# Performance work log

Hardware: AMD Instinct MI355X
Metric: run time of the kernel (lower is better)

Reference implementation:

```python
import jax, jax.numpy as jnp
import numpy as np

BITS = 4
PACK = 32 // BITS  # 8 nibbles per int32
GROUP = 128
MASK = (1 << BITS) - 1


def _dequant(qweight, qzeros, scales):
    # qweight: [K//8, N] int32, nibbles packed along K (input) dim
    # qzeros : [G, N//8] int32, nibbles packed along N (output) dim
    # scales : [G, N] float
    shifts = jnp.arange(PACK, dtype=jnp.int32) * BITS  # [8]
    Kp, N = qweight.shape
    G = scales.shape[0]
    # unpack weights along input dim -> [K, N]
    w = (qweight[:, None, :] >> shifts[None, :, None]) & MASK  # [K//8, 8, N]
    w = w.reshape(Kp * PACK, N).astype(scales.dtype)
    # unpack zeros along output dim -> [G, N]
    z = (qzeros[:, :, None] >> shifts[None, None, :]) & MASK  # [G, N//8, 8]
    z = z.reshape(G, N).astype(scales.dtype) + 1.0  # GPTQ +1 zero offset
    # broadcast per-group zero/scale over GROUP consecutive input rows
    z_full = jnp.repeat(z, GROUP, axis=0)       # [K, N]
    s_full = jnp.repeat(scales, GROUP, axis=0)  # [K, N]
    return (w - z_full) * s_full  # [K, N]


def setup_inputs() -> dict:
    key = jax.random.key(0)
    k1, k2, k3, k4 = jax.random.split(key, 4)
    K, N, T = 4096, 11008, 8192
    x = jax.random.normal(k1, (T, K), dtype=jnp.float32)
    qweight = jax.random.randint(k2, (K // PACK, N), 0, 2147483647, dtype=jnp.int32)
    qzeros = jax.random.randint(k3, (K // GROUP, N // PACK), 0, 2147483647, dtype=jnp.int32)
    scales = jax.random.uniform(k4, (K // GROUP, N), dtype=jnp.float32) * 0.01
    return {"x": x, "qweight": qweight, "qzeros": qzeros, "scales": scales}


def reference(x, qweight, qzeros, scales):
    W = _dequant(qweight, qzeros, scales)  # [K, N]
    return x @ W  # [T, N]
```

## Files before the change

### kernel.cpp

```cpp
#include <hip/hip_runtime.h>
#include <hip/hip_bf16.h>
#include <cstdint>
#include <cstddef>


#define K_DIM 4096
#define N_DIM 11008
#define GROUP_SZ 128
#define KB (K_DIM * 2)
#define NTILES_K (K_DIM / 64)

typedef __bf16 bf16x8_t __attribute__((ext_vector_type(8)));
typedef float f32x4_t __attribute__((ext_vector_type(4)));

__device__ __forceinline__ void async_copy16(const void* g, void* l) {
    __builtin_amdgcn_global_load_lds((const __attribute__((address_space(1))) void*)g,
                                     (__attribute__((address_space(3))) void*)l,
                                     16, 0, 0);
}

__global__ __launch_bounds__(256) void convert_x_kernel(const float* __restrict__ x,
                                                        __bf16* __restrict__ xb,
                                                        long total,
                                                        unsigned* __restrict__ counter) {
    if (counter && blockIdx.x == 0 && threadIdx.x == 0) counter[0] = 0u;
    long i = ((long)blockIdx.x * 256 + threadIdx.x) * 8;
    if (i >= total) return;
    const float4* p = (const float4*)(x + i);
    float4 u = p[0], v = p[1];
    bf16x8_t o;
    o[0] = (__bf16)u.x; o[1] = (__bf16)u.y; o[2] = (__bf16)u.z; o[3] = (__bf16)u.w;
    o[4] = (__bf16)v.x; o[5] = (__bf16)v.y; o[6] = (__bf16)v.z; o[7] = (__bf16)v.w;
    *(bf16x8_t*)(xb + i) = o;
}

__global__ __launch_bounds__(256) void dequant_kernel(const int* __restrict__ qw,
                                                      const int* __restrict__ qz,
                                                      const float* __restrict__ sc,
                                                      __bf16* __restrict__ Wt) {
    __shared__ __align__(16) __bf16 dqT[128 * 136];
    __shared__ float dqS[128];
    __shared__ float dqB[128];
    const int n0 = blockIdx.x * 128;
    const int g  = blockIdx.y;
    const int t  = threadIdx.x;

    if (t < 128) {
        int n = n0 + t;
        float s = sc[(size_t)g * N_DIM + n];
        int z = (qz[(size_t)g * (N_DIM / 8) + (n >> 3)] >> ((n & 7) * 4)) & 15;
        dqS[t] = s;
        dqB[t] = -(float)(z + 1) * s;
    }
    __syncthreads();

#pragma unroll
    for (int it = 0; it < 8; ++it) {
        int wi  = it * 256 + t;
        int row = wi >> 7;
        int col = wi & 127;
        int q = qw[(size_t)(g * 16 + row) * N_DIM + n0 + col];
        float s = dqS[col], b = dqB[col];
        bf16x8_t v;
#pragma unroll
        for (int j = 0; j < 8; ++j) {
            float w = (float)((q >> (4 * j)) & 15);
            v[j] = (__bf16)fmaf(w, s, b);
        }
        *(bf16x8_t*)(&dqT[col * 136 + row * 8]) = v;
    }
    __syncthreads();

    int n_loc = t & 127, half = t >> 7;
    const __bf16* src = &dqT[n_loc * 136 + half * 64];
    __bf16* dst = Wt + (size_t)(n0 + n_loc) * K_DIM + g * GROUP_SZ + half * 64;
#pragma unroll
    for (int i = 0; i < 8; ++i)
        *(bf16x8_t*)(dst + i * 8) = *(const bf16x8_t*)(src + i * 8);
}

__device__ __forceinline__ void map_tile(int vid, int mtiles, int ntiles,
                                         int& mt, int& nt) {
    if ((mtiles & 15) == 0) {
        const int bandsz = 16 * ntiles;
        const int band = vid / bandsz, rem = vid % bandsz;
        nt = rem >> 4;
        mt = (band << 4) + (rem & 15);
    } else {
        mt = vid % mtiles;
        nt = vid / mtiles;
    }
}

__global__ __launch_bounds__(512, 2) void gemm256_kernel(const __bf16* __restrict__ A,
                                                         const __bf16* __restrict__ Bt,
                                                         float* __restrict__ C,
                                                         int mtiles, int ntiles,
                                                         unsigned* counter, int ntotal) {
    __shared__ __align__(16) char ldsA[2][256 * 128];
    __shared__ __align__(16) char ldsB[2][256 * 128];
    __shared__ int sVid;
    const int tid = threadIdx.x;

    int srcA[2], srcB[2], dstA[2], dstB[2];
#pragma unroll
    for (int q = 0; q < 2; ++q) {
        const int f = q * 512 + tid;
        const int r = f >> 3, c = f & 7;
        const int swz = (c * 16) ^ ((r & 7) << 4);
        const int Ra = r + (r & 64);
        const int Rb = r + (r & ~31);
        srcA[q] = Ra * KB + swz;  dstA[q] = Ra * 128 + c * 16;
        srcB[q] = Rb * KB + swz;  dstB[q] = Rb * 128 + c * 16;
    }

    const int lane = tid & 63;
    const int wid = tid >> 6;
    const int wm = wid >> 2, wn = wid & 3;
    const int lr = lane & 15, lq = lane >> 4;
    const int kOff0 = (lq * 16) ^ ((lr & 7) << 4);
    const int kOff1 = (64 + lq * 16) ^ ((lr & 7) << 4);
    const int aRowBase = wm * 128 + lr;
    const int bRowBase = wn * 64 + lr;

    bf16x8_t aF[4][2], bF[4][2];
    f32x4_t acc[8][4];

#define GL_A(AP, KT, BUFS, ROFF) do {                                                      \
    async_copy16((AP) + (size_t)(KT) * 128 + (ROFF) * KB + srcA[0],                        \
                 &ldsA[BUFS][(ROFF) * 128] + dstA[0]);                                     \
    async_copy16((AP) + (size_t)(KT) * 128 + (ROFF) * KB + srcA[1],                        \
                 &ldsA[BUFS][(ROFF) * 128] + dstA[1]);                                     \
} while (0)
#define GL_B(BP, KT, BUFS, ROFF) do {                                                      \
    async_copy16((BP) + (size_t)(KT) * 128 + (ROFF) * KB + srcB[0],                        \
                 &ldsB[BUFS][(ROFF) * 128] + dstB[0]);                                     \
    async_copy16((BP) + (size_t)(KT) * 128 + (ROFF) * KB + srcB[1],                        \
                 &ldsB[BUFS][(ROFF) * 128] + dstB[1]);                                     \
} while (0)
#define READ_A(MQ, BUFC) do {                                                              \
    _Pragma("unroll") for (int i = 0; i < 4; ++i) {                                        \
        const char* _p = &ldsA[BUFC][(aRowBase + (MQ) * 64 + i * 16) * 128];               \
        aF[i][0] = *(const bf16x8_t*)(_p + kOff0);                                         \
        aF[i][1] = *(const bf16x8_t*)(_p + kOff1);                                         \
    }                                                                                      \
} while (0)
#define READ_B(NQ, BUFC) do {                                                              \
    _Pragma("unroll") for (int j = 0; j < 2; ++j) {                                        \
        const char* _p = &ldsB[BUFC][(bRowBase + ((NQ) * 2 + j) * 16) * 128];              \
        bF[(NQ) * 2 + j][0] = *(const bf16x8_t*)(_p + kOff0);                              \
        bF[(NQ) * 2 + j][1] = *(const bf16x8_t*)(_p + kOff1);                              \
    }                                                                                      \
} while (0)
#define MFMA_QUAD(MQ, NQ) do {                                                             \
    _Pragma("unroll") for (int kk = 0; kk < 2; ++kk)                                       \
    _Pragma("unroll") for (int i = 0; i < 4; ++i)                                          \
    _Pragma("unroll") for (int j = 0; j < 2; ++j)                                          \
        acc[(MQ) * 4 + i][(NQ) * 2 + j] = __builtin_amdgcn_mfma_f32_16x16x32_bf16(         \
            aF[i][kk], bF[(NQ) * 2 + j][kk], acc[(MQ) * 4 + i][(NQ) * 2 + j], 0, 0, 0);    \
} while (0)
#define BARRIER() asm volatile("s_barrier" ::: "memory")
#define VMCNT4()  asm volatile("s_waitcnt vmcnt(4)" ::: "memory")
#define VMCNT0()  asm volatile("s_waitcnt vmcnt(0)" ::: "memory")

#define KTILE(AP, BP, BUFC, KTS) do {                                                      \
    READ_A(0, BUFC); READ_B(0, BUFC);                                                      \
    GL_A(AP, KTS, (BUFC) ^ 1, 0);                                                          \
    VMCNT4(); BARRIER();                                                                   \
    MFMA_QUAD(0, 0);                                                                       \
    READ_B(1, BUFC);                                                                       \
    GL_B(BP, KTS, (BUFC) ^ 1, 0);                                                          \
    VMCNT4(); BARRIER();                                                                   \
    MFMA_QUAD(0, 1);                                                                       \
    READ_A(1, BUFC);                                                                       \
    GL_B(BP, KTS, (BUFC) ^ 1, 32);                                                         \
    BARRIER();                                                                             \
    MFMA_QUAD(1, 1);                                                                       \
    GL_A(AP, KTS, (BUFC) ^ 1, 64);                                                         \
    VMCNT4(); BARRIER();                                                                   \
    MFMA_QUAD(1, 0);                                                                       \
} while (0)

#define KTILE_LAST(NAP, NBP, HAVE) do {                                                    \
    READ_A(0, 1); READ_B(0, 1);                                                            \
    if (HAVE) { GL_A(NAP, 0, 0, 0); VMCNT4(); } else { VMCNT0(); }                         \
    BARRIER();                                                                             \
    MFMA_QUAD(0, 0);                                                                       \
    READ_B(1, 1);                                                                          \
    if (HAVE) GL_B(NBP, 0, 0, 0);                                                          \
    VMCNT4(); BARRIER();                                                                   \
    MFMA_QUAD(0, 1);                                                                       \
    READ_A(1, 1);                                                                          \
    if (HAVE) GL_B(NBP, 0, 0, 32);                                                         \
    BARRIER();                                                                             \
    MFMA_QUAD(1, 1);                                                                       \
    if (HAVE) GL_A(NAP, 0, 0, 64);                                                         \
    VMCNT4(); BARRIER();                                                                   \
    MFMA_QUAD(1, 0);                                                                       \
} while (0)

    int vid;
    if (counter) {
        if (tid == 0) sVid = (int)atomicAdd(counter, 1u);
        __syncthreads();
        vid = sVid;
    } else {
        const int nwg = gridDim.x, bid = blockIdx.x;
        vid = (nwg & 7) ? bid : ((bid & 7) * (nwg >> 3) + (bid >> 3));
    }

    bool first = true;
    while (vid < ntotal) {
        int mt, nt;
        map_tile(vid, mtiles, ntiles, mt, nt);
        const char* aPanel = (const char*)A + (size_t)mt * 256 * KB;
        const char* bPanel = (const char*)Bt + (size_t)nt * 256 * KB;

        if (first) {
            GL_A(aPanel, 0, 0, 0); GL_B(bPanel, 0, 0, 0);
            GL_B(bPanel, 0, 0, 32); GL_A(aPanel, 0, 0, 64);
            VMCNT4(); BARRIER();
            first = false;
        }

#pragma unroll
        for (int m = 0; m < 8; ++m)
#pragma unroll
            for (int n = 0; n < 4; ++n)
                acc[m][n] = (f32x4_t){0.f, 0.f, 0.f, 0.f};

#pragma unroll 1
        for (int kt = 0; kt < NTILES_K - 2; kt += 2) {
            KTILE(aPanel, bPanel, 0, kt + 1);
            KTILE(aPanel, bPanel, 1, kt + 2);
        }
        KTILE(aPanel, bPanel, 0, NTILES_K - 1);

        int nvid;
        if (counter) {
            if (tid == 0) sVid = (int)atomicAdd(counter, 1u);
            __syncthreads();
            nvid = sVid;
        } else {
            nvid = ntotal;
        }
        const bool have = nvid < ntotal;
        const char* naP = aPanel;
        const char* nbP = bPanel;
        if (have) {
            int nmt, nnt;
            map_tile(nvid, mtiles, ntiles, nmt, nnt);
            naP = (const char*)A + (size_t)nmt * 256 * KB;
            nbP = (const char*)Bt + (size_t)nnt * 256 * KB;
        }
        KTILE_LAST(naP, nbP, have);

#pragma unroll
        for (int m = 0; m < 8; ++m) {
            const size_t gr = (size_t)mt * 256 + wm * 128 + m * 16 + lq * 4;
#pragma unroll
            for (int n = 0; n < 4; ++n) {
                const size_t gc = (size_t)nt * 256 + wn * 64 + n * 16 + lr;
                float* cp = C + gr * N_DIM + gc;
#pragma unroll
                for (int rg = 0; rg < 4; ++rg)
                    cp[(size_t)rg * N_DIM] = acc[m][n][rg];
            }
        }

        vid = nvid;
    }
}

__global__ __launch_bounds__(256) void fallback_kernel(const float* __restrict__ x,
                                                       const int* __restrict__ qw,
                                                       const int* __restrict__ qz,
                                                       const float* __restrict__ sc,
                                                       float* __restrict__ out) {
    __shared__ float xrow[K_DIM];
    const int t = blockIdx.y;
    const int n = blockIdx.x * 256 + threadIdx.x;
    for (int i = threadIdx.x; i < K_DIM; i += 256)
        xrow[i] = x[(size_t)t * K_DIM + i];
    __syncthreads();
    if (n >= N_DIM) return;
    float acc = 0.f;
    for (int g = 0; g < K_DIM / GROUP_SZ; ++g) {
        float s = sc[(size_t)g * N_DIM + n];
        int z = (qz[(size_t)g * (N_DIM / 8) + (n >> 3)] >> ((n & 7) * 4)) & 15;
        float b = -(float)(z + 1) * s;
        for (int kp = g * 16; kp < g * 16 + 16; ++kp) {
            int q = qw[(size_t)kp * N_DIM + n];
#pragma unroll
            for (int j = 0; j < 8; ++j) {
                float w = (float)((q >> (4 * j)) & 15);
                acc = fmaf(xrow[kp * 8 + j], fmaf(w, s, b), acc);
            }
        }
    }
    out[(size_t)t * N_DIM + n] = acc;
}

extern "C" void kernel_launch(void* const* d_in, const int* in_sizes, int n_in,
                              void* d_out, int out_size, void* d_ws, size_t ws_size,
                              hipStream_t stream) {
    const float* x  = (const float*)d_in[0];
    const int*   qw = (const int*)d_in[1];
    const int*   qz = (const int*)d_in[2];
    const float* sc = (const float*)d_in[3];
    float* out = (float*)d_out;

    const long T = (long)in_sizes[0] / K_DIM;
    const size_t xb_bytes = (size_t)T * K_DIM * sizeof(__bf16);
    const size_t wt_bytes = (size_t)N_DIM * K_DIM * sizeof(__bf16);
    const size_t cnt_off  = (xb_bytes + wt_bytes + 255) & ~(size_t)255;

    if (ws_size >= xb_bytes + wt_bytes && (T % 256) == 0) {
        __bf16* xb = (__bf16*)d_ws;
        __bf16* Wt = (__bf16*)((char*)d_ws + xb_bytes);
        unsigned* counter = (ws_size >= cnt_off + 256)
                          ? (unsigned*)((char*)d_ws + cnt_off) : nullptr;
        long total = T * K_DIM;
        long nthr = total / 8;
        convert_x_kernel<<<dim3((unsigned)((nthr + 255) / 256)), dim3(256), 0, stream>>>(x, xb, total, counter);
        dequant_kernel<<<dim3(N_DIM / 128, K_DIM / GROUP_SZ), dim3(256), 0, stream>>>(qw, qz, sc, Wt);
        const int mtiles = (int)(T / 256);
        const int ntiles = N_DIM / 256;
        const int ntotal = mtiles * ntiles;
        const unsigned grid = counter ? 256u : (unsigned)ntotal;
        gemm256_kernel<<<dim3(grid), dim3(512), 0, stream>>>(xb, Wt, out, mtiles, ntiles, counter, ntotal);
    } else {
        fallback_kernel<<<dim3(N_DIM / 256 + 1, (unsigned)T), dim3(256), 0, stream>>>(x, qw, qz, sc, out);
    }
}
```

Baseline: 729.0 us.

## Double-buffer MFMA fragments and prefetch next k-tile fragments across tile boundary

Splits the A/B register fragments into separate low/high and b0/b1 sets so LDS reads for the next quadrant, and for the next k-tile's first quadrant, are issued before the current MFMA block rather than after a barrier. This hides LDS read latency behind MFMA work and reorders the quadrant sequence to (0,0),(0,1),(1,0),(1,1). In exchange it raises VGPR use, which risks spills or lower occupancy, and it changes barrier/vmcnt placement, including a weaker wait in the last tile.

```diff
diff --git a/kernel.cpp b/kernel.cpp
--- a/kernel.cpp
+++ b/kernel.cpp
@@ -123,7 +123,7 @@
     const int aRowBase = wm * 128 + lr;
     const int bRowBase = wn * 64 + lr;
 
-    bf16x8_t aF[4][2], bF[4][2];
+    bf16x8_t aLo[4][2], aHi[4][2], b0[2][2], b1[2][2];
     f32x4_t acc[8][4];
 
 #define GL_A(AP, KT, BUFS, ROFF) do {                                                      \
@@ -138,65 +138,70 @@
     async_copy16((BP) + (size_t)(KT) * 128 + (ROFF) * KB + srcB[1],                        \
                  &ldsB[BUFS][(ROFF) * 128] + dstB[1]);                                     \
 } while (0)
-#define READ_A(MQ, BUFC) do {                                                              \
+#define READ_AX(DST, MQ, BUF) do {                                                         \
     _Pragma("unroll") for (int i = 0; i < 4; ++i) {                                        \
-        const char* _p = &ldsA[BUFC][(aRowBase + (MQ) * 64 + i * 16) * 128];               \
-        aF[i][0] = *(const bf16x8_t*)(_p + kOff0);                                         \
-        aF[i][1] = *(const bf16x8_t*)(_p + kOff1);                                         \
+        const char* _p = &ldsA[BUF][(aRowBase + (MQ) * 64 + i * 16) * 128];                \
+        DST[i][0] = *(const bf16x8_t*)(_p + kOff0);                                        \
+        DST[i][1] = *(const bf16x8_t*)(_p + kOff1);                                        \
     }                                                                                      \
 } while (0)
-#define READ_B(NQ, BUFC) do {                                                              \
+#define READ_BX(DST, NQ, BUF) do {                                                         \
     _Pragma("unroll") for (int j = 0; j < 2; ++j) {                                        \
-        const char* _p = &ldsB[BUFC][(bRowBase + ((NQ) * 2 + j) * 16) * 128];              \
-        bF[(NQ) * 2 + j][0] = *(const bf16x8_t*)(_p + kOff0);                              \
-        bF[(NQ) * 2 + j][1] = *(const bf16x8_t*)(_p + kOff1);                              \
+        const char* _p = &ldsB[BUF][(bRowBase + ((NQ) * 2 + j) * 16) * 128];               \
+        DST[j][0] = *(const bf16x8_t*)(_p + kOff0);                                        \
+        DST[j][1] = *(const bf16x8_t*)(_p + kOff1);                                        \
     }                                                                                      \
 } while (0)
-#define MFMA_QUAD(MQ, NQ) do {                                                             \
+#define MFMA_Q(AARR, BARR, MQ, NQ) do {                                                    \
     _Pragma("unroll") for (int kk = 0; kk < 2; ++kk)                                       \
     _Pragma("unroll") for (int i = 0; i < 4; ++i)                                          \
     _Pragma("unroll") for (int j = 0; j < 2; ++j)                                          \
         acc[(MQ) * 4 + i][(NQ) * 2 + j] = __builtin_amdgcn_mfma_f32_16x16x32_bf16(         \
-            aF[i][kk], bF[(NQ) * 2 + j][kk], acc[(MQ) * 4 + i][(NQ) * 2 + j], 0, 0, 0);    \
+            AARR[i][kk], BARR[j][kk], acc[(MQ) * 4 + i][(NQ) * 2 + j], 0, 0, 0);           \
 } while (0)
 #define BARRIER() asm volatile("s_barrier" ::: "memory")
 #define VMCNT4()  asm volatile("s_waitcnt vmcnt(4)" ::: "memory")
+#define VMCNT2()  asm volatile("s_waitcnt vmcnt(2)" ::: "memory")
 #define VMCNT0()  asm volatile("s_waitcnt vmcnt(0)" ::: "memory")
 
 #define KTILE(AP, BP, BUFC, KTS) do {                                                      \
-    READ_A(0, BUFC); READ_B(0, BUFC);                                                      \
+                                                                                   \
     GL_A(AP, KTS, (BUFC) ^ 1, 0);                                                          \
-    VMCNT4(); BARRIER();                                                                   \
-    MFMA_QUAD(0, 0);                                                                       \
-    READ_B(1, BUFC);                                                                       \
+    VMCNT4(); BARRIER();                                              \
+    READ_BX(b1, 1, BUFC);                                                                  \
+    MFMA_Q(aLo, b0, 0, 0);                                                                 \
+                                                                                   \
     GL_B(BP, KTS, (BUFC) ^ 1, 0);                                                          \
-    VMCNT4(); BARRIER();                                                                   \
-    MFMA_QUAD(0, 1);                                                                       \
-    READ_A(1, BUFC);                                                                       \
+    VMCNT4(); BARRIER();                                              \
+    READ_AX(aHi, 1, BUFC);                                                                 \
+    MFMA_Q(aLo, b1, 0, 1);                                                                 \
+                                                              \
     GL_B(BP, KTS, (BUFC) ^ 1, 32);                                                         \
+    MFMA_Q(aHi, b0, 1, 0);                                                                 \
+                                                                                   \
+    GL_A(AP, KTS, (BUFC) ^ 1, 64);                                                         \
+    VMCNT4(); BARRIER();                                         \
+    READ_AX(aLo, 0, (BUFC) ^ 1);                                                           \
+    READ_BX(b0, 0, (BUFC) ^ 1);                                                            \
+    MFMA_Q(aHi, b1, 1, 1);                                                                 \
+} while (0)
+
+#define KTILE_LAST(NAP, NBP, HAVE) do {                                                    \
+    if (HAVE) { GL_A(NAP, 0, 0, 0); VMCNT4(); } else { VMCNT2(); }                         \
     BARRIER();                                                                             \
-    MFMA_QUAD(1, 1);                                                                       \
-    GL_A(AP, KTS, (BUFC) ^ 1, 64);                                                         \
-    VMCNT4(); BARRIER();                                                                   \
-    MFMA_QUAD(1, 0);                                                                       \
-} while (0)
-
-#define KTILE_LAST(NAP, NBP, HAVE) do {                                                    \
-    READ_A(0, 1); READ_B(0, 1);                                                            \
-    if (HAVE) { GL_A(NAP, 0, 0, 0); VMCNT4(); } else { VMCNT0(); }                         \
+    READ_BX(b1, 1, 1);                                                                     \
+    MFMA_Q(aLo, b0, 0, 0);                                                                 \
+    if (HAVE) { GL_B(NBP, 0, 0, 0); VMCNT4(); } else { VMCNT0(); }                         \
     BARRIER();                                                                             \
-    MFMA_QUAD(0, 0);                                                                       \
-    READ_B(1, 1);                                                                          \
-    if (HAVE) GL_B(NBP, 0, 0, 0);                                                          \
-    VMCNT4(); BARRIER();                                                                   \
-    MFMA_QUAD(0, 1);                                                                       \
-    READ_A(1, 1);                                                                          \
+    READ_AX(aHi, 1, 1);                                                                    \
+    MFMA_Q(aLo, b1, 0, 1);                                                                 \
     if (HAVE) GL_B(NBP, 0, 0, 32);                                                         \
+    MFMA_Q(aHi, b0, 1, 0);                                                                 \
+    if (HAVE) { GL_A(NAP, 0, 0, 64); VMCNT4(); }                                           \
     BARRIER();                                                                             \
-    MFMA_QUAD(1, 1);                                                                       \
-    if (HAVE) GL_A(NAP, 0, 0, 64);                                                         \
-    VMCNT4(); BARRIER();                                                                   \
-    MFMA_QUAD(1, 0);                                                                       \
+    READ_AX(aLo, 0, 0);                                                                    \
+    READ_BX(b0, 0, 0);                                                                     \
+    MFMA_Q(aHi, b1, 1, 1);                                                                 \
 } while (0)
 
     int vid;
@@ -220,6 +225,8 @@
             GL_A(aPanel, 0, 0, 0); GL_B(bPanel, 0, 0, 0);
             GL_B(bPanel, 0, 0, 32); GL_A(aPanel, 0, 0, 64);
             VMCNT4(); BARRIER();
+            READ_AX(aLo, 0, 0);
+            READ_BX(b0, 0, 0);
             first = false;
         }
 
```

Result: slower. 830.7 us (+14.0%).
